# Performance work log

Hardware: AMD Instinct MI355X
Metric: run time of the kernel (lower is better)

The kernel has to match this reference:

```python
import jax, jax.numpy as jnp
import numpy as np

DIM = 512
HEADS = 8
DIM_HEAD = 64
SCALE = DIM_HEAD ** -0.5


def setup_inputs() -> dict:
    key = jax.random.key(0)
    ks = jax.random.split(key, 4)
    b, n = 4, 2048
    x = jax.random.normal(ks[0], (b, n, DIM), dtype=jnp.float32)
    Wq = jax.random.normal(ks[1], (DIM, HEADS * DIM_HEAD), dtype=jnp.float32) * (DIM ** -0.5)
    Wkv = jax.random.normal(ks[2], (DIM, 2 * HEADS * DIM_HEAD), dtype=jnp.float32) * (DIM ** -0.5)
    Wo = jax.random.normal(ks[3], (HEADS * DIM_HEAD, DIM), dtype=jnp.float32) * ((HEADS * DIM_HEAD) ** -0.5)
    bo = jnp.zeros((DIM,), dtype=jnp.float32)
    return {"x": x, "Wq": Wq, "Wkv": Wkv, "Wo": Wo, "bo": bo}


def reference(x, Wq, Wkv, Wo, bo):
    b, n, _ = x.shape
    # context = x (self-attention path, kv_include_self=False)
    q = x @ Wq                      # [b, n, h*d]
    kv = x @ Wkv                    # [b, n, 2*h*d]
    k, v = jnp.split(kv, 2, axis=-1)

    def split_heads(t):
        return t.reshape(b, n, HEADS, DIM_HEAD).transpose(0, 2, 1, 3)  # [b,h,n,d]

    q, k, v = split_heads(q), split_heads(k), split_heads(v)
    dots = jnp.einsum('bhid,bhjd->bhij', q, k) * SCALE  # [b,h,n,n]
    attn = jax.nn.softmax(dots, axis=-1)
    out = jnp.einsum('bhij,bhjd->bhid', attn, v)        # [b,h,n,d]
    out = out.transpose(0, 2, 1, 3).reshape(b, n, HEADS * DIM_HEAD)
    return out @ Wo + bo
```

## Files before the change

### kernel.cpp

```cpp
#include <hip/hip_runtime.h>
#include <hip/hip_bf16.h>

typedef short bf16x8 __attribute__((ext_vector_type(8)));
typedef float fx4    __attribute__((ext_vector_type(4)));

#if __has_builtin(__builtin_amdgcn_exp2f)
#define EXP2 __builtin_amdgcn_exp2f
#else
#define EXP2 exp2f
#endif

__device__ __forceinline__ unsigned pk2(float a, float b) {
  union { __hip_bfloat162 h; unsigned u; } cv;
  cv.h = __float22bfloat162_rn(float2{a, b});
  return cv.u;
}
__device__ __forceinline__ uint2 pk4(const fx4& v) {
  uint2 r;
  r.x = pk2(v[0], v[1]);
  r.y = pk2(v[2], v[3]);
  return r;
}

__device__ __forceinline__ void gld16(const void* g, void* l) {
  __builtin_amdgcn_global_load_lds(
      (const __attribute__((address_space(1))) unsigned int*)g,
      (__attribute__((address_space(3))) unsigned int*)l, 16, 0, 0);
}

__global__ __launch_bounds__(256) void cvt_x_kernel(const float* __restrict__ x,
                                                    short* __restrict__ xb, int n4) {
  int i = blockIdx.x * blockDim.x + threadIdx.x;
  if (i < n4) {
    const float4 s = *(const float4*)(x + (size_t)i * 4);
    uint2 o; o.x = pk2(s.x, s.y); o.y = pk2(s.z, s.w);
    *(uint2*)(xb + (size_t)i * 4) = o;
  }
}

__global__ __launch_bounds__(256) void prep_w_kernel(const float* __restrict__ Wq,
                                                     const float* __restrict__ Wkv,
                                                     const float* __restrict__ Wo,
                                                     short* __restrict__ WallT,
                                                     short* __restrict__ WoT,
                                                     float qscale) {
  __shared__ float t[32][33];
  const int bx = blockIdx.x;
  const bool mode0 = bx < 48;
  const int ct = (mode0 ? bx : bx - 48) * 32, kt = blockIdx.y * 32;
  const int tx = threadIdx.x, ty = threadIdx.y;
  short* outT = mode0 ? WallT : WoT;
#pragma unroll
  for (int s = 0; s < 4; ++s) {
    int k = kt + ty + s * 8;
    int c = ct + tx;
    float v;
    if (mode0) v = (c < 512) ? Wq[(size_t)k * 512 + c] * qscale
                             : Wkv[(size_t)k * 1024 + (c - 512)];
    else       v = Wo[(size_t)k * 512 + c];
    t[ty + s * 8][tx] = v;
  }
  __syncthreads();
#pragma unroll
  for (int s = 0; s < 4; ++s) {
    int c = ct + ty + s * 8;
    int k = kt + tx;
    unsigned u = __float_as_uint(t[tx][ty + s * 8]);
    u = (u + 0x7fffu + ((u >> 16) & 1u)) >> 16;
    outT[(size_t)c * 512 + k] = (short)u;
  }
}

__global__ __launch_bounds__(256) void gemm_qkv(
    const short* __restrict__ A, const short* __restrict__ Bt,
    short* __restrict__ oq, short* __restrict__ ok, short* __restrict__ ovT) {
  __shared__ short As[2 * 128 * 32];
  __shared__ short Bs[2 * 128 * 32];
  const int K = 512;
  const int tid = threadIdx.x;
  const int wave = tid >> 6, lane = tid & 63;
  const int quad = lane >> 4, l15 = lane & 15;
  const int wm = wave >> 1, wn = wave & 1;
  const int m0 = blockIdx.y * 128, n0 = blockIdx.x * 128;
  const bool swapped = (n0 < 1024);

  fx4 acc[4][4];
#pragma unroll
  for (int i = 0; i < 4; ++i)
#pragma unroll
    for (int j = 0; j < 4; ++j) acc[i][j] = fx4{0.f, 0.f, 0.f, 0.f};

  for (int k0 = 0; k0 < K; k0 += 64) {
#pragma unroll
    for (int c = 0; c < 4; ++c) {
      int u = c * 256 + tid;
      int slab = u >> 9, r2 = u & 511;
      int row = r2 >> 2, seg = r2 & 3;
      gld16(A  + (size_t)(m0 + row) * K + k0 + slab * 32 + seg * 8,
            As + (size_t)(c * 256 + wave * 64) * 8);
      gld16(Bt + (size_t)(n0 + row) * K + k0 + slab * 32 + seg * 8,
            Bs + (size_t)(c * 256 + wave * 64) * 8);
    }
    __syncthreads();
#pragma unroll
    for (int ks2 = 0; ks2 < 2; ++ks2) {
      bf16x8 af[4], bfr[4];
#pragma unroll
      for (int i = 0; i < 4; ++i)
        af[i] = *(const bf16x8*)(As + ks2 * 4096 + (wm * 64 + i * 16 + l15) * 32 + quad * 8);
#pragma unroll
      for (int i = 0; i < 4; ++i)
        bfr[i] = *(const bf16x8*)(Bs + ks2 * 4096 + (wn * 64 + i * 16 + l15) * 32 + quad * 8);
      if (swapped) {
#pragma unroll
        for (int mi = 0; mi < 4; ++mi)
#pragma unroll
          for (int ni = 0; ni < 4; ++ni)
            acc[mi][ni] = __builtin_amdgcn_mfma_f32_16x16x32_bf16(bfr[ni], af[mi], acc[mi][ni], 0, 0, 0);
      } else {
#pragma unroll
        for (int mi = 0; mi < 4; ++mi)
#pragma unroll
          for (int ni = 0; ni < 4; ++ni)
            acc[mi][ni] = __builtin_amdgcn_mfma_f32_16x16x32_bf16(af[mi], bfr[ni], acc[mi][ni], 0, 0, 0);
      }
    }
    __syncthreads();
  }

  const int rowb = m0 + wm * 64;
  const int colb = n0 + wn * 64;
  const int cls = n0 >> 9;
  if (cls < 2) {
    short* base = (cls == 0) ? oq : ok;
#pragma unroll
    for (int mi = 0; mi < 4; ++mi) {
      int t = rowb + mi * 16 + l15;
      int bb = t >> 11, ii = t & 2047;
#pragma unroll
      for (int ni = 0; ni < 4; ++ni) {
        int f = (colb + ni * 16 + quad * 4) & 511;
        int hh = f >> 6, dd = f & 63;
        *(uint2*)(base + ((size_t)(bb * 8 + hh) * 2048 + ii) * 64 + dd) = pk4(acc[mi][ni]);
      }
    }
  } else {
#pragma unroll
    for (int mi = 0; mi < 4; ++mi) {
      int rbase = rowb + mi * 16 + quad * 4;
      int bb = rbase >> 11;
      int ii = rbase & 2047;
#pragma unroll
      for (int ni = 0; ni < 4; ++ni) {
        int c = (colb + ni * 16 + l15) & 511;
        int hh = c >> 6, dd = c & 63;
        *(uint2*)(ovT + ((size_t)(bb * 8 + hh) * 64 + dd) * 2048 + ii) = pk4(acc[mi][ni]);
      }
    }
  }
}

__global__ __launch_bounds__(256) void gemm_out(
    const short* __restrict__ A, const short* __restrict__ Bt,
    float* __restrict__ of, const float* __restrict__ bias) {
  __shared__ short As[2 * 64 * 32];
  __shared__ short Bs[2 * 128 * 32];
  const int K = 512, N = 512;
  const int tid = threadIdx.x;
  const int wave = tid >> 6, lane = tid & 63;
  const int quad = lane >> 4, l15 = lane & 15;
  const int wm = wave >> 1, wn = wave & 1;
  const int m0 = blockIdx.y * 64, n0 = blockIdx.x * 128;

  fx4 acc[2][4];
#pragma unroll
  for (int i = 0; i < 2; ++i)
#pragma unroll
    for (int j = 0; j < 4; ++j) acc[i][j] = fx4{0.f, 0.f, 0.f, 0.f};

  for (int k0 = 0; k0 < K; k0 += 64) {
#pragma unroll
    for (int c = 0; c < 2; ++c) {
      int u = c * 256 + tid;
      int slab = u >> 8, r2 = u & 255;
      int row = r2 >> 2, seg = r2 & 3;
      gld16(A + (size_t)(m0 + row) * K + k0 + slab * 32 + seg * 8,
            As + (size_t)(c * 256 + wave * 64) * 8);
    }
#pragma unroll
    for (int c = 0; c < 4; ++c) {
      int u = c * 256 + tid;
      int slab = u >> 9, r2 = u & 511;
      int row = r2 >> 2, seg = r2 & 3;
      gld16(Bt + (size_t)(n0 + row) * K + k0 + slab * 32 + seg * 8,
            Bs + (size_t)(c * 256 + wave * 64) * 8);
    }
    __syncthreads();
#pragma unroll
    for (int ks2 = 0; ks2 < 2; ++ks2) {
      bf16x8 af[2], bfr[4];
#pragma unroll
      for (int i = 0; i < 2; ++i)
        af[i] = *(const bf16x8*)(As + ks2 * 2048 + (wm * 32 + i * 16 + l15) * 32 + quad * 8);
#pragma unroll
      for (int i = 0; i < 4; ++i)
        bfr[i] = *(const bf16x8*)(Bs + ks2 * 4096 + (wn * 64 + i * 16 + l15) * 32 + quad * 8);
#pragma unroll
      for (int mi = 0; mi < 2; ++mi)
#pragma unroll
        for (int ni = 0; ni < 4; ++ni)
          acc[mi][ni] = __builtin_amdgcn_mfma_f32_16x16x32_bf16(af[mi], bfr[ni], acc[mi][ni], 0, 0, 0);
    }
    __syncthreads();
  }

  const int rowb = m0 + wm * 32;
  const int colb = n0 + wn * 64;
#pragma unroll
  for (int mi = 0; mi < 2; ++mi)
#pragma unroll
    for (int ni = 0; ni < 4; ++ni) {
      int cg = colb + ni * 16 + l15;
      float bv = bias[cg];
#pragma unroll
      for (int r = 0; r < 4; ++r) {
        int rg = rowb + mi * 16 + quad * 4 + r;
        of[(size_t)rg * N + cg] = acc[mi][ni][r] + bv;
      }
    }
}

__global__ __launch_bounds__(256) void attn_kernel(
    const short* __restrict__ Q, const short* __restrict__ K,
    const short* __restrict__ Vt, short* __restrict__ O) {
  __shared__ short Ks[128 * 64];
  __shared__ short Vs[64 * 128];
  __shared__ short Ps[4 * 16 * 136];

  const int tid = threadIdx.x;
  const int wave = tid >> 6, lane = tid & 63;
  const int quad = lane >> 4, l15 = lane & 15;
  const int bh = blockIdx.y;
  const int b = bh >> 3, h = bh & 7;
  const int i0 = blockIdx.x * 64 + wave * 16;
  short* Pw = Ps + wave * (16 * 136);

  bf16x8 qf[2];
#pragma unroll
  for (int ks = 0; ks < 2; ++ks)
    qf[ks] = *(const bf16x8*)(Q + ((size_t)bh * 2048 + i0 + l15) * 64 + ks * 32 + quad * 8);

  fx4 oacc[4];
  float l_s = 0.f;
#pragma unroll
  for (int dt = 0; dt < 4; ++dt) oacc[dt] = fx4{0.f, 0.f, 0.f, 0.f};

  for (int j0 = 0; j0 < 2048; j0 += 128) {
#pragma unroll
    for (int t = 0; t < 4; ++t) {
      int idx = t * 256 + tid;
      int rowK = idx >> 3;
      int sgK = (idx & 7) ^ (rowK & 7);
      gld16(K + ((size_t)bh * 2048 + j0 + rowK) * 64 + sgK * 8,
            Ks + (size_t)(t * 256 + wave * 64) * 8);
      int rowV = idx >> 4;
      int sgV = (idx & 15) ^ (rowV & 15);
      gld16(Vt + ((size_t)bh * 64 + rowV) * 2048 + j0 + sgV * 8,
            Vs + (size_t)(t * 256 + wave * 64) * 8);
    }
    __syncthreads();

    fx4 s[8];
#pragma unroll
    for (int jt = 0; jt < 8; ++jt) s[jt] = fx4{0.f, 0.f, 0.f, 0.f};
#pragma unroll
    for (int ks = 0; ks < 2; ++ks) {
#pragma unroll
      for (int jt = 0; jt < 8; ++jt) {
        bf16x8 kf = *(const bf16x8*)(Ks + (jt * 16 + l15) * 64 + (((ks * 4 + quad) ^ (l15 & 7)) * 8));
        s[jt] = __builtin_amdgcn_mfma_f32_16x16x32_bf16(kf, qf[ks], s[jt], 0, 0, 0);
      }
    }

#pragma unroll
    for (int jt = 0; jt < 8; ++jt)
#pragma unroll
      for (int r = 0; r < 4; ++r) s[jt][r] = EXP2(s[jt][r]);
    fx4 t0 = s[0] + s[1], t1 = s[2] + s[3], t2 = s[4] + s[5], t3 = s[6] + s[7];
    fx4 u0 = t0 + t1, u1 = t2 + t3;
    fx4 u = u0 + u1;
    l_s += (u[0] + u[1]) + (u[2] + u[3]);
#pragma unroll
    for (int jt = 0; jt < 8; ++jt)
      *(uint2*)(Pw + l15 * 136 + jt * 16 + quad * 4) = pk4(s[jt]);

#pragma unroll
    for (int kj = 0; kj < 4; ++kj) {
      bf16x8 pf = *(const bf16x8*)(Pw + l15 * 136 + kj * 32 + quad * 8);
#pragma unroll
      for (int dt = 0; dt < 4; ++dt) {
        bf16x8 vf = *(const bf16x8*)(Vs + (dt * 16 + l15) * 128 + (((kj * 4 + quad) ^ l15) * 8));
        oacc[dt] = __builtin_amdgcn_mfma_f32_16x16x32_bf16(vf, pf, oacc[dt], 0, 0, 0);
      }
    }
    __syncthreads();
  }

  l_s += __shfl_xor(l_s, 16);
  l_s += __shfl_xor(l_s, 32);
  float inv = __builtin_amdgcn_rcpf(l_s);

  size_t rowbase = ((size_t)b * 2048 + i0 + l15) * 512 + h * 64;
#pragma unroll
  for (int dt = 0; dt < 4; ++dt) {
    fx4 o = oacc[dt] * inv;
    *(uint2*)(O + rowbase + dt * 16 + quad * 4) = pk4(o);
  }
}

extern "C" void kernel_launch(void* const* d_in, const int* in_sizes, int n_in,
                              void* d_out, int out_size, void* d_ws, size_t ws_size,
                              hipStream_t stream) {
  const float* x   = (const float*)d_in[0];
  const float* Wq  = (const float*)d_in[1];
  const float* Wkv = (const float*)d_in[2];
  const float* Wo  = (const float*)d_in[3];
  const float* bo  = (const float*)d_in[4];
  float* out = (float*)d_out;

  char* p = (char*)d_ws;
  short* xb    = (short*)p; p += (size_t)8192 * 512 * 2;
  short* WallT = (short*)p; p += (size_t)1536 * 512 * 2;
  short* WoT   = (short*)p; p += (size_t)512 * 512 * 2;
  short* qb    = (short*)p; p += (size_t)32 * 2048 * 64 * 2;
  short* kb    = (short*)p; p += (size_t)32 * 2048 * 64 * 2;
  short* vTb   = (short*)p; p += (size_t)32 * 64 * 2048 * 2;
  short* Ob    = (short*)p; p += (size_t)8192 * 512 * 2;

  const float qscale = 0.125f * 1.4426950408889634f;

  cvt_x_kernel<<<4096, 256, 0, stream>>>(x, xb, 1048576);
  prep_w_kernel<<<dim3(64, 16), dim3(32, 8), 0, stream>>>(Wq, Wkv, Wo, WallT, WoT, qscale);
  gemm_qkv<<<dim3(12, 64), 256, 0, stream>>>(xb, WallT, qb, kb, vTb);
  attn_kernel<<<dim3(32, 32), 256, 0, stream>>>(qb, kb, vTb, Ob);
  gemm_out<<<dim3(4, 128), 256, 0, stream>>>(Ob, WoT, out, bo);
}
```

Baseline: 181.7 us.

## Register-prefetch K/V tiles with smaller 64-key blocks and MFMA row sums

The attention kernel switches from direct global-to-LDS loads of 128-key tiles to register prefetching of the next 64-key tile while the current tile is computed, double-buffered through registers. Tile size and LDS footprint are halved, which may raise occupancy. The softmax denominator is now accumulated with an MFMA against a ones vector instead of fp32 adds and cross-lane shuffles. This adds MFMA work and, since the sum now uses bf16-rounded probabilities, slightly changes numerics; the last iteration issues a wasted wrap-around prefetch.

```diff
diff --git a/kernel.cpp b/kernel.cpp
--- a/kernel.cpp
+++ b/kernel.cpp
@@ -233,9 +233,9 @@
 __global__ __launch_bounds__(256) void attn_kernel(
     const short* __restrict__ Q, const short* __restrict__ K,
     const short* __restrict__ Vt, short* __restrict__ O) {
-  __shared__ short Ks[128 * 64];
-  __shared__ short Vs[64 * 128];
-  __shared__ short Ps[4 * 16 * 136];
+  __shared__ short Ks[64 * 64];
+  __shared__ short Vs[64 * 64];
+  __shared__ short Ps[4 * 16 * 72];
 
   const int tid = threadIdx.x;
   const int wave = tid >> 6, lane = tid & 63;
@@ -243,72 +243,83 @@
   const int bh = blockIdx.y;
   const int b = bh >> 3, h = bh & 7;
   const int i0 = blockIdx.x * 64 + wave * 16;
-  short* Pw = Ps + wave * (16 * 136);
+  short* Pw = Ps + wave * (16 * 72);
+
+  const int idx0 = tid, idx1 = 256 + tid;
+  const int row0 = idx0 >> 3, sg0 = (idx0 & 7) ^ (row0 & 7);
+  const int row1 = idx1 >> 3, sg1 = (idx1 & 7) ^ (row1 & 7);
+  const short* Kb = K + (size_t)bh * 2048 * 64;
+  const short* Vb = Vt + (size_t)bh * 64 * 2048;
 
   bf16x8 qf[2];
 #pragma unroll
   for (int ks = 0; ks < 2; ++ks)
     qf[ks] = *(const bf16x8*)(Q + ((size_t)bh * 2048 + i0 + l15) * 64 + ks * 32 + quad * 8);
 
+  bf16x8 ones;
+#pragma unroll
+  for (int c = 0; c < 8; ++c) ones[c] = (short)0x3F80;
+
   fx4 oacc[4];
-  float l_s = 0.f;
+  fx4 acc_l = fx4{0.f, 0.f, 0.f, 0.f};
 #pragma unroll
   for (int dt = 0; dt < 4; ++dt) oacc[dt] = fx4{0.f, 0.f, 0.f, 0.f};
 
-  for (int j0 = 0; j0 < 2048; j0 += 128) {
-#pragma unroll
-    for (int t = 0; t < 4; ++t) {
-      int idx = t * 256 + tid;
-      int rowK = idx >> 3;
-      int sgK = (idx & 7) ^ (rowK & 7);
-      gld16(K + ((size_t)bh * 2048 + j0 + rowK) * 64 + sgK * 8,
-            Ks + (size_t)(t * 256 + wave * 64) * 8);
-      int rowV = idx >> 4;
-      int sgV = (idx & 15) ^ (rowV & 15);
-      gld16(Vt + ((size_t)bh * 64 + rowV) * 2048 + j0 + sgV * 8,
-            Vs + (size_t)(t * 256 + wave * 64) * 8);
-    }
-    __syncthreads();
-
-    fx4 s[8];
-#pragma unroll
-    for (int jt = 0; jt < 8; ++jt) s[jt] = fx4{0.f, 0.f, 0.f, 0.f};
+  bf16x8 kpre0, kpre1, vpre0, vpre1;
+  {
+    kpre0 = *(const bf16x8*)(Kb + (size_t)row0 * 64 + sg0 * 8);
+    kpre1 = *(const bf16x8*)(Kb + (size_t)row1 * 64 + sg1 * 8);
+    vpre0 = *(const bf16x8*)(Vb + (size_t)row0 * 2048 + sg0 * 8);
+    vpre1 = *(const bf16x8*)(Vb + (size_t)row1 * 2048 + sg1 * 8);
+  }
+
+  for (int j0 = 0; j0 < 2048; j0 += 64) {
+    __syncthreads();
+    *(bf16x8*)(Ks + idx0 * 8) = kpre0;
+    *(bf16x8*)(Ks + idx1 * 8) = kpre1;
+    *(bf16x8*)(Vs + idx0 * 8) = vpre0;
+    *(bf16x8*)(Vs + idx1 * 8) = vpre1;
+    {
+      int jn = (j0 + 64) & 2047;
+      kpre0 = *(const bf16x8*)(Kb + (size_t)(jn + row0) * 64 + sg0 * 8);
+      kpre1 = *(const bf16x8*)(Kb + (size_t)(jn + row1) * 64 + sg1 * 8);
+      vpre0 = *(const bf16x8*)(Vb + (size_t)row0 * 2048 + jn + sg0 * 8);
+      vpre1 = *(const bf16x8*)(Vb + (size_t)row1 * 2048 + jn + sg1 * 8);
+    }
+    __syncthreads();
+
+    fx4 s[4];
+#pragma unroll
+    for (int jt = 0; jt < 4; ++jt) s[jt] = fx4{0.f, 0.f, 0.f, 0.f};
 #pragma unroll
     for (int ks = 0; ks < 2; ++ks) {
 #pragma unroll
-      for (int jt = 0; jt < 8; ++jt) {
+      for (int jt = 0; jt < 4; ++jt) {
         bf16x8 kf = *(const bf16x8*)(Ks + (jt * 16 + l15) * 64 + (((ks * 4 + quad) ^ (l15 & 7)) * 8));
         s[jt] = __builtin_amdgcn_mfma_f32_16x16x32_bf16(kf, qf[ks], s[jt], 0, 0, 0);
       }
     }
 
 #pragma unroll
-    for (int jt = 0; jt < 8; ++jt)
+    for (int jt = 0; jt < 4; ++jt) {
 #pragma unroll
       for (int r = 0; r < 4; ++r) s[jt][r] = EXP2(s[jt][r]);
-    fx4 t0 = s[0] + s[1], t1 = s[2] + s[3], t2 = s[4] + s[5], t3 = s[6] + s[7];
-    fx4 u0 = t0 + t1, u1 = t2 + t3;
-    fx4 u = u0 + u1;
-    l_s += (u[0] + u[1]) + (u[2] + u[3]);
-#pragma unroll
-    for (int jt = 0; jt < 8; ++jt)
-      *(uint2*)(Pw + l15 * 136 + jt * 16 + quad * 4) = pk4(s[jt]);
-
-#pragma unroll
-    for (int kj = 0; kj < 4; ++kj) {
-      bf16x8 pf = *(const bf16x8*)(Pw + l15 * 136 + kj * 32 + quad * 8);
+      *(uint2*)(Pw + l15 * 72 + jt * 16 + quad * 4) = pk4(s[jt]);
+    }
+
+#pragma unroll
+    for (int kj = 0; kj < 2; ++kj) {
+      bf16x8 pf = *(const bf16x8*)(Pw + l15 * 72 + kj * 32 + quad * 8);
+      acc_l = __builtin_amdgcn_mfma_f32_16x16x32_bf16(ones, pf, acc_l, 0, 0, 0);
 #pragma unroll
       for (int dt = 0; dt < 4; ++dt) {
-        bf16x8 vf = *(const bf16x8*)(Vs + (dt * 16 + l15) * 128 + (((kj * 4 + quad) ^ l15) * 8));
+        bf16x8 vf = *(const bf16x8*)(Vs + (dt * 16 + l15) * 64 + (((kj * 4 + quad) ^ (l15 & 7)) * 8));
         oacc[dt] = __builtin_amdgcn_mfma_f32_16x16x32_bf16(vf, pf, oacc[dt], 0, 0, 0);
       }
     }
-    __syncthreads();
-  }
-
-  l_s += __shfl_xor(l_s, 16);
-  l_s += __shfl_xor(l_s, 32);
-  float inv = __builtin_amdgcn_rcpf(l_s);
+  }
+
+  float inv = __builtin_amdgcn_rcpf(acc_l[0]);
 
   size_t rowbase = ((size_t)b * 2048 + i0 + l15) * 512 + h * 64;
 #pragma unroll
```

Result: no change. 181.1 us (-0.3%).
